# Optimization experiments

Measured on AMD Instinct MI355X. Metric: run time of the kernel, lower is better.

Reference implementation:

```python
import jax, jax.numpy as jnp
import numpy as np

LATENT = 512
VOCAB = 32000
START_TOKEN = 0
END_TOKEN = 1
BATCH = 128
BN_EPS = 1e-5


def setup_inputs() -> dict:
    key = jax.random.key(0)
    k = jax.random.split(key, 10)
    s = 0.02
    L, V = LATENT, VOCAB
    return {
        "z": jax.random.normal(k[0], (BATCH, L), dtype=jnp.float32),
        "emb": jax.random.normal(k[1], (V, L), dtype=jnp.float32) * s,      # embedding table
        "Wp1": jax.random.normal(k[2], (2 * L, L), dtype=jnp.float32) * s,  # project layer 1
        "bp1": jnp.zeros((2 * L,), jnp.float32),
        "Wp2": jax.random.normal(k[3], (2 * L, 2 * L), dtype=jnp.float32) * s,  # project layer 2
        "bp2": jnp.zeros((2 * L,), jnp.float32),
        "Wih": jax.random.normal(k[4], (4 * L, L), dtype=jnp.float32) * s,  # LSTMCell input weights (i,f,g,o)
        "Whh": jax.random.normal(k[5], (4 * L, L), dtype=jnp.float32) * s,
        "bih": jnp.zeros((4 * L,), jnp.float32),
        "bhh": jnp.zeros((4 * L,), jnp.float32),
        "Wo1": jax.random.normal(k[6], (2 * L, L), dtype=jnp.float32) * s,  # output MLP layer 1
        "bo1": jnp.zeros((2 * L,), jnp.float32),
        "bn_g": jnp.ones((2 * L,), jnp.float32),   # BatchNorm1d (eval mode)
        "bn_b": jnp.zeros((2 * L,), jnp.float32),
        "bn_m": jnp.zeros((2 * L,), jnp.float32),
        "bn_v": jnp.ones((2 * L,), jnp.float32),
        "Wo2": jax.random.normal(k[7], (V - 1, 2 * L), dtype=jnp.float32) * s,  # vocab head
        "bo2": jnp.zeros((V - 1,), jnp.float32),
        "max_len": 50,
    }


def _elu01(x):
    # nn.ELU(alpha=0.1)
    return jnp.where(x > 0, x, 0.1 * (jnp.exp(x) - 1.0))


def _run(z, emb, Wp1, bp1, Wp2, bp2, Wih, Whh, bih, bhh,
         Wo1, bo1, bn_g, bn_b, bn_m, bn_v, Wo2, bo2, max_len):
    B, L = z.shape
    # project z -> (h, c); dropout inactive in eval mode
    h1 = jax.nn.relu(z @ Wp1.T + bp1)
    hc = _elu01(h1 @ Wp2.T + bp2)
    h, c = jnp.split(hc, 2, axis=1)            # each [B, L]
    e0 = jnp.broadcast_to(emb[START_TOKEN], (B, L))
    keys = jax.random.split(jax.random.key(42), max_len)
    inv_std = bn_g / jnp.sqrt(bn_v + BN_EPS)   # fused BN scale (eval)

    def step(carry, key):
        h, c, e = carry
        gates = e @ Wih.T + bih + h @ Whh.T + bhh
        i, f, g, o = jnp.split(gates, 4, axis=1)  # torch LSTMCell gate order
        c = jax.nn.sigmoid(f) * c + jax.nn.sigmoid(i) * jnp.tanh(g)
        h = jax.nn.sigmoid(o) * jnp.tanh(c)
        a = jax.nn.relu(h) @ Wo1.T + bo1
        a = (a - bn_m) * inv_std + bn_b
        logits = jax.nn.relu(a) @ Wo2.T + bo2      # [B, V-1]
        logp = jax.nn.log_softmax(logits, axis=-1)
        # Categorical sampling via Gumbel-max
        sample = jnp.argmax(logits + jax.random.gumbel(key, logits.shape), axis=-1)
        lp = jnp.take_along_axis(logp, sample[:, None], axis=1)[:, 0]
        ent = -jnp.sum(jnp.exp(logp) * logp, axis=-1)
        return (h, c, jnp.take(emb, sample, axis=0)), (sample, lp, ent)

    _, (xs, lps, ents) = jax.lax.scan(step, (h, c, e0), keys)
    x = xs.T          # [B, T]
    lps = lps.T       # [B, T]
    ents = ents.T     # [B, T]
    # first END occurrence (argmax returns first max; replicates torch semantics incl. its length-1 quirk)
    end_pos = jnp.argmax((x == END_TOKEN).astype(jnp.float32), axis=1)
    seq_len = end_pos + 1
    seq_len = jnp.where(seq_len == 1, max_len, seq_len)
    mask = jnp.arange(max_len)[None, :] < seq_len[:, None]
    x_out = jnp.where(mask, x + 1, 0)                      # pad_sequence(padding=-1) then +1 -> 0 pad
    lp_out = jnp.where(mask, lps, 0.0)                     # padded per-step log-probs
    ent_mean = jnp.sum(jnp.where(mask, ents, 0.0), axis=1) / seq_len.astype(ents.dtype)
    return x_out, lp_out, ent_mean


def reference(z, emb, Wp1, bp1, Wp2, bp2, Wih, Whh, bih, bhh,
              Wo1, bo1, bn_g, bn_b, bn_m, bn_v, Wo2, bo2, max_len):
    return _run(z, emb, Wp1, bp1, Wp2, bp2, Wih, Whh, bih, bhh,
                Wo1, bo1, bn_g, bn_b, bn_m, bn_v, Wo2, bo2, max_len)
```

## Files before the change

kernel.cpp:

```cpp
#include <hip/hip_runtime.h>
#include <stdint.h>
#include <math.h>

#define BATCH  128
#define NV     31999
#define NSTEP  50
#define NPB    500
#define TINYF  1.17549435e-38f

typedef __attribute__((ext_vector_type(8))) short bf16x8;
typedef __attribute__((ext_vector_type(4))) float f32x4;
typedef __attribute__((ext_vector_type(4))) unsigned int u32x4;

__host__ __device__ __forceinline__ void tf2x32(uint32_t k0, uint32_t k1,
                                                uint32_t x0, uint32_t x1,
                                                uint32_t& o0, uint32_t& o1) {
  uint32_t k2 = k0 ^ k1 ^ 0x1BD11BDAu;
  x0 += k0; x1 += k1;
#define TF_R(r) { x0 += x1; x1 = (x1 << (r)) | (x1 >> (32 - (r))); x1 ^= x0; }
  TF_R(13) TF_R(15) TF_R(26) TF_R(6)
  x0 += k1; x1 += k2 + 1u;
  TF_R(17) TF_R(29) TF_R(16) TF_R(24)
  x0 += k2; x1 += k0 + 2u;
  TF_R(13) TF_R(15) TF_R(26) TF_R(6)
  x0 += k0; x1 += k1 + 3u;
  TF_R(17) TF_R(29) TF_R(16) TF_R(24)
  x0 += k1; x1 += k2 + 4u;
  TF_R(13) TF_R(15) TF_R(26) TF_R(6)
  x0 += k2; x1 += k0 + 5u;
#undef TF_R
  o0 = x0; o1 = x1;
}

__device__ __forceinline__ float sigm(float x) { return 1.0f / (1.0f + expf(-x)); }

__device__ __forceinline__ float gumbelv(uint32_t k0, uint32_t k1, uint32_t f) {
  uint32_t o0, o1; tf2x32(k0, k1, 0u, f, o0, o1);
  uint32_t bits = o0 ^ o1;
  float ff = __uint_as_float((bits >> 9) | 0x3f800000u) - 1.0f;
  float u = ff + TINYF;
  return -logf(-logf(u));
}

__device__ __forceinline__ unsigned short bfhi(float x) {
  uint32_t u = __float_as_uint(x);
  u += 0x7fffu + ((u >> 16) & 1u);
  return (unsigned short)(u >> 16);
}
__device__ __forceinline__ void split2(float x, unsigned short& h, unsigned short& l) {
  unsigned short hh = bfhi(x);
  float hf = __uint_as_float(((uint32_t)hh) << 16);
  h = hh; l = bfhi(x - hf);
}

#define MFMA3(ah, al, bh, bl, c)                                            \
  c = __builtin_amdgcn_mfma_f32_16x16x32_bf16(ah, bh, c, 0, 0, 0);          \
  c = __builtin_amdgcn_mfma_f32_16x16x32_bf16(ah, bl, c, 0, 0, 0);          \
  c = __builtin_amdgcn_mfma_f32_16x16x32_bf16(al, bh, c, 0, 0, 0);

__global__ __launch_bounds__(256) void gemm_part(
    const float* __restrict__ A, int lda,
    const float* __restrict__ Wa, const float* __restrict__ Wb,
    int ks, int K, int N, int KC, float* __restrict__ part)
{
  __shared__ float As[32][132];
  __shared__ float Ws[32][68];
  const int tx = threadIdx.x;
  const int n0 = blockIdx.x * 64;
  const int kc = blockIdx.y;
  const int cg = tx & 15, rg = tx >> 4;
  float acc[8][4] = {};
  const int kend = (kc + 1) * KC;
  for (int kk = kc * KC; kk < kend; kk += 32) {
    __syncthreads();
#pragma unroll
    for (int i = 0; i < 16; ++i) {
      int e = tx + 256 * i; int b = e >> 5, k = e & 31;
      As[k][b] = A[b * lda + kk + k];
    }
#pragma unroll
    for (int i = 0; i < 8; ++i) {
      int e = tx + 256 * i; int n = e >> 5, k = e & 31;
      int nn = n0 + n, kg = kk + k;
      float w;
      if (kg < ks) w = Wa[(size_t)nn * ks + kg];
      else         w = Wb[(size_t)nn * (K - ks) + (kg - ks)];
      Ws[k][n] = w;
    }
    __syncthreads();
#pragma unroll
    for (int k = 0; k < 32; ++k) {
      float4 a0 = *(const float4*)&As[k][rg * 8];
      float4 a1 = *(const float4*)&As[k][rg * 8 + 4];
      float4 wv = *(const float4*)&Ws[k][cg * 4];
      float ar[8] = {a0.x, a0.y, a0.z, a0.w, a1.x, a1.y, a1.z, a1.w};
      float wr[4] = {wv.x, wv.y, wv.z, wv.w};
#pragma unroll
      for (int r = 0; r < 8; ++r)
#pragma unroll
        for (int c = 0; c < 4; ++c) acc[r][c] += ar[r] * wr[c];
    }
  }
  size_t base = (size_t)kc * BATCH * N;
#pragma unroll
  for (int r = 0; r < 8; ++r) {
    int row = rg * 8 + r;
    float4 v4 = make_float4(acc[r][0], acc[r][1], acc[r][2], acc[r][3]);
    *(float4*)&part[base + (size_t)row * N + n0 + cg * 4] = v4;
  }
}

__global__ void k_reduce_relu(const float* __restrict__ part, int nkc,
                              const float* __restrict__ bias,
                              float* __restrict__ out, int N) {
  int i = blockIdx.x * 256 + threadIdx.x;
  int n = i % N;
  float s = bias[n];
  for (int kc = 0; kc < nkc; ++kc) s += part[(size_t)kc * BATCH * N + i];
  out[i] = fmaxf(s, 0.0f);
}

__global__ void k_reduce_elu_split(const float* __restrict__ part, int nkc,
                                   const float* __restrict__ bias,
                                   unsigned short* __restrict__ xh,
                                   unsigned short* __restrict__ xl,
                                   float* __restrict__ cbuf) {
  int i = blockIdx.x * 256 + threadIdx.x;
  int b = i >> 10, n = i & 1023;
  float s = bias[n];
  for (int kc = 0; kc < nkc; ++kc) s += part[(size_t)kc * BATCH * 1024 + i];
  float e = (s > 0.0f) ? s : 0.1f * (expf(s) - 1.0f);
  if (n < 512) {
    unsigned short h_, l_; split2(e, h_, l_);
    xh[b * 1024 + 512 + n] = h_; xl[b * 1024 + 512 + n] = l_;
  } else cbuf[b * 512 + (n - 512)] = e;
}

__global__ void k_fill_e0(const float* __restrict__ emb,
                          unsigned short* __restrict__ xh,
                          unsigned short* __restrict__ xl) {
  int i = blockIdx.x * 256 + threadIdx.x;
  int b = i >> 9, k = i & 511;
  unsigned short h_, l_; split2(emb[k], h_, l_);
  xh[b * 1024 + k] = h_; xl[b * 1024 + k] = l_;
}

__global__ void k_prep_gates(const float* __restrict__ Wih, const float* __restrict__ Whh,
                             const float* __restrict__ bih, const float* __restrict__ bhh,
                             unsigned short* __restrict__ Wh, unsigned short* __restrict__ Wl,
                             float* __restrict__ bg) {
  int i = blockIdx.x * 256 + threadIdx.x;
  int idx8 = i * 8;
  int n = idx8 >> 10, k0 = idx8 & 1023;
  const float* src = (k0 < 512) ? (Wih + (size_t)n * 512 + k0)
                                : (Whh + (size_t)n * 512 + (k0 - 512));
  float4 a = *(const float4*)src, b = *(const float4*)(src + 4);
  float wv[8] = {a.x, a.y, a.z, a.w, b.x, b.y, b.z, b.w};
  unsigned short hh[8], ll[8];
#pragma unroll
  for (int q = 0; q < 8; ++q) split2(wv[q], hh[q], ll[q]);
  u32x4 h4, l4;
#pragma unroll
  for (int q = 0; q < 4; ++q) {
    h4[q] = (uint32_t)hh[2 * q] | ((uint32_t)hh[2 * q + 1] << 16);
    l4[q] = (uint32_t)ll[2 * q] | ((uint32_t)ll[2 * q + 1] << 16);
  }
  *(u32x4*)(Wh + (size_t)idx8) = h4;
  *(u32x4*)(Wl + (size_t)idx8) = l4;
  if (i < 256) {
#pragma unroll
    for (int q = 0; q < 8; ++q) bg[i * 8 + q] = bih[i * 8 + q] + bhh[i * 8 + q];
  }
}

__global__ void k_prep_out1(const float* __restrict__ Wo1, const float* __restrict__ bo1,
                            const float* __restrict__ g, const float* __restrict__ bb,
                            const float* __restrict__ m, const float* __restrict__ v,
                            unsigned short* __restrict__ Wh, unsigned short* __restrict__ Wl,
                            float* __restrict__ S, float* __restrict__ T) {
  int i = blockIdx.x * 256 + threadIdx.x;
  int idx8 = i * 8;
  float4 a = *(const float4*)(Wo1 + idx8), b = *(const float4*)(Wo1 + idx8 + 4);
  float wv[8] = {a.x, a.y, a.z, a.w, b.x, b.y, b.z, b.w};
  unsigned short hh[8], ll[8];
#pragma unroll
  for (int q = 0; q < 8; ++q) split2(wv[q], hh[q], ll[q]);
  u32x4 h4, l4;
#pragma unroll
  for (int q = 0; q < 4; ++q) {
    h4[q] = (uint32_t)hh[2 * q] | ((uint32_t)hh[2 * q + 1] << 16);
    l4[q] = (uint32_t)ll[2 * q] | ((uint32_t)ll[2 * q + 1] << 16);
  }
  *(u32x4*)(Wh + (size_t)idx8) = h4;
  *(u32x4*)(Wl + (size_t)idx8) = l4;
  if (i < 128) {
#pragma unroll
    for (int q = 0; q < 8; ++q) {
      int n = i * 8 + q;
      float s = g[n] / sqrtf(v[n] + 1e-5f);
      S[n] = s;
      T[n] = (bo1[n] - m[n]) * s + bb[n];
    }
  }
}

__global__ void k_prep_wo2(const float* __restrict__ W,
                           unsigned short* __restrict__ Wh, unsigned short* __restrict__ Wl,
                           int total8) {
  int i = blockIdx.x * 256 + threadIdx.x;
  if (i >= total8) return;
  const float* wp = W + (size_t)i * 8;
  float4 a = *(const float4*)wp, b = *(const float4*)(wp + 4);
  float wv[8] = {a.x, a.y, a.z, a.w, b.x, b.y, b.z, b.w};
  unsigned short hh[8], ll[8];
#pragma unroll
  for (int q = 0; q < 8; ++q) split2(wv[q], hh[q], ll[q]);
  u32x4 h4, l4;
#pragma unroll
  for (int q = 0; q < 4; ++q) {
    h4[q] = (uint32_t)hh[2 * q] | ((uint32_t)hh[2 * q + 1] << 16);
    l4[q] = (uint32_t)ll[2 * q] | ((uint32_t)ll[2 * q + 1] << 16);
  }
  *(u32x4*)(Wh + (size_t)i * 8) = h4;
  *(u32x4*)(Wl + (size_t)i * 8) = l4;
}

__global__ __launch_bounds__(256) void k_gates(
    const unsigned short* __restrict__ Ah, const unsigned short* __restrict__ Al,
    const unsigned short* __restrict__ Wh, const unsigned short* __restrict__ Wl,
    const float* __restrict__ bg, float* __restrict__ cbuf,
    unsigned short* __restrict__ xh, unsigned short* __restrict__ xl,
    unsigned short* __restrict__ rhh, unsigned short* __restrict__ rhl)
{
  __shared__ __align__(16) unsigned char SM[40960];
  unsigned short (*WHb)[2][64][40] = (unsigned short(*)[2][64][40])SM;
  unsigned short (*WLb)[2][64][40] = (unsigned short(*)[2][64][40])(SM + 20480);
  const int tx = threadIdx.x;
  const int lane = tx & 63, w = tx >> 6;
  const int l15 = lane & 15, g4 = lane >> 4;
  const int gblk = blockIdx.x;
  const int arow0 = w * 32 + l15, ak = g4 * 8;
  const int sr = tx >> 2, sq = tx & 3;
  const int grow = (sr >> 4) * 512 + gblk * 16 + (sr & 15);
  const size_t wbase = (size_t)grow * 1024;

  f32x4 acc[2][4] = {};
  u32x4 RH[2][2], RL[2][2];
  bf16x8 QH[2][2][2], QL[2][2][2];

  auto ldW = [&](int set, int t) {
    const int kk = t * 64 + sq * 16;
    RH[set][0] = *(const u32x4*)(Wh + wbase + kk);
    RH[set][1] = *(const u32x4*)(Wh + wbase + kk + 8);
    RL[set][0] = *(const u32x4*)(Wl + wbase + kk);
    RL[set][1] = *(const u32x4*)(Wl + wbase + kk + 8);
  };
  auto stW = [&](int set, int buf) {
    const int kc = sq >> 1, ko = (sq & 1) * 16;
    *(u32x4*)&WHb[buf][kc][sr][ko]     = RH[set][0];
    *(u32x4*)&WHb[buf][kc][sr][ko + 8] = RH[set][1];
    *(u32x4*)&WLb[buf][kc][sr][ko]     = RL[set][0];
    *(u32x4*)&WLb[buf][kc][sr][ko + 8] = RL[set][1];
  };
  auto ldA = [&](int set, int t) {
#pragma unroll
    for (int rf = 0; rf < 2; ++rf)
#pragma unroll
      for (int kc = 0; kc < 2; ++kc) {
        size_t ao = (size_t)(arow0 + rf * 16) * 1024 + t * 64 + kc * 32 + ak;
        QH[set][rf][kc] = *(const bf16x8*)(Ah + ao);
        QL[set][rf][kc] = *(const bf16x8*)(Al + ao);
      }
  };
  auto comp = [&](int buf, int set) {
#pragma unroll
    for (int kc = 0; kc < 2; ++kc)
#pragma unroll
      for (int cf = 0; cf < 4; ++cf) {
        int col = cf * 16 + l15;
        bf16x8 bh = *(const bf16x8*)&WHb[buf][kc][col][ak];
        bf16x8 bl = *(const bf16x8*)&WLb[buf][kc][col][ak];
#pragma unroll
        for (int rf = 0; rf < 2; ++rf) { MFMA3(QH[set][rf][kc], QL[set][rf][kc], bh, bl, acc[rf][cf]); }
      }
  };

  ldW(0, 0); ldW(1, 1); ldA(0, 0);
  stW(0, 0); __syncthreads();
  for (int t = 0; t < 16; ++t) {
    const int pb = t & 1;
    if (t < 14) ldW(pb, t + 2);
    if (t < 15) ldA(pb ^ 1, t + 1);
    comp(pb, pb);
    if (t < 15) stW(pb ^ 1, pb ^ 1);
    __syncthreads();
  }
  float* gex = (float*)SM;
#pragma unroll
  for (int rf = 0; rf < 2; ++rf)
#pragma unroll
    for (int cf = 0; cf < 4; ++cf)
#pragma unroll
      for (int r = 0; r < 4; ++r) {
        int brow = w * 32 + rf * 16 + g4 * 4 + r;
        gex[(cf * 128 + brow) * 17 + l15] = acc[rf][cf][r];
      }
  __syncthreads();
#pragma unroll
  for (int i = 0; i < 8; ++i) {
    int e = tx + 256 * i;
    int b = e >> 4, lj = e & 15;
    int jg = gblk * 16 + lj;
    float gi = gex[(0 * 128 + b) * 17 + lj] + bg[jg];
    float gf = gex[(1 * 128 + b) * 17 + lj] + bg[512 + jg];
    float gg = gex[(2 * 128 + b) * 17 + lj] + bg[1024 + jg];
    float go = gex[(3 * 128 + b) * 17 + lj] + bg[1536 + jg];
    float co = cbuf[b * 512 + jg];
    float cn = sigm(gf) * co + sigm(gi) * tanhf(gg);
    float hn = sigm(go) * tanhf(cn);
    cbuf[b * 512 + jg] = cn;
    unsigned short h_, l_;
    split2(hn, h_, l_);
    xh[b * 1024 + 512 + jg] = h_; xl[b * 1024 + 512 + jg] = l_;
    float r = fmaxf(hn, 0.0f);
    split2(r, h_, l_);
    rhh[b * 512 + jg] = h_; rhl[b * 512 + jg] = l_;
  }
}

__global__ __launch_bounds__(256) void k_out1(
    const unsigned short* __restrict__ Ah, const unsigned short* __restrict__ Al,
    const unsigned short* __restrict__ Wh, const unsigned short* __restrict__ Wl,
    const float* __restrict__ S, const float* __restrict__ T,
    unsigned short* __restrict__ r2h, unsigned short* __restrict__ r2l)
{
  __shared__ __align__(16) unsigned char SM[40960];
  unsigned short (*WHb)[2][64][40] = (unsigned short(*)[2][64][40])SM;
  unsigned short (*WLb)[2][64][40] = (unsigned short(*)[2][64][40])(SM + 20480);
  const int tx = threadIdx.x;
  const int lane = tx & 63, w = tx >> 6;
  const int l15 = lane & 15, g4 = lane >> 4;
  const int n0 = blockIdx.x * 64;
  const int arow0 = w * 32 + l15, ak = g4 * 8;
  const int sr = tx >> 2, sq = tx & 3;
  const size_t wbase = (size_t)(n0 + sr) * 512;

  f32x4 acc[2][4] = {};
  u32x4 RH[2][2], RL[2][2];
  bf16x8 QH[2][2][2], QL[2][2][2];

  auto ldW = [&](int set, int t) {
    const int kk = t * 64 + sq * 16;
    RH[set][0] = *(const u32x4*)(Wh + wbase + kk);
    RH[set][1] = *(const u32x4*)(Wh + wbase + kk + 8);
    RL[set][0] = *(const u32x4*)(Wl + wbase + kk);
    RL[set][1] = *(const u32x4*)(Wl + wbase + kk + 8);
  };
  auto stW = [&](int set, int buf) {
    const int kc = sq >> 1, ko = (sq & 1) * 16;
    *(u32x4*)&WHb[buf][kc][sr][ko]     = RH[set][0];
    *(u32x4*)&WHb[buf][kc][sr][ko + 8] = RH[set][1];
    *(u32x4*)&WLb[buf][kc][sr][ko]     = RL[set][0];
    *(u32x4*)&WLb[buf][kc][sr][ko + 8] = RL[set][1];
  };
  auto ldA = [&](int set, int t) {
#pragma unroll
    for (int rf = 0; rf < 2; ++rf)
#pragma unroll
      for (int kc = 0; kc < 2; ++kc) {
        size_t ao = (size_t)(arow0 + rf * 16) * 512 + t * 64 + kc * 32 + ak;
        QH[set][rf][kc] = *(const bf16x8*)(Ah + ao);
        QL[set][rf][kc] = *(const bf16x8*)(Al + ao);
      }
  };
  auto comp = [&](int buf, int set) {
#pragma unroll
    for (int kc = 0; kc < 2; ++kc)
#pragma unroll
      for (int cf = 0; cf < 4; ++cf) {
        int col = cf * 16 + l15;
        bf16x8 bh = *(const bf16x8*)&WHb[buf][kc][col][ak];
        bf16x8 bl = *(const bf16x8*)&WLb[buf][kc][col][ak];
#pragma unroll
        for (int rf = 0; rf < 2; ++rf) { MFMA3(QH[set][rf][kc], QL[set][rf][kc], bh, bl, acc[rf][cf]); }
      }
  };

  ldW(0, 0); ldW(1, 1); ldA(0, 0);
  stW(0, 0); __syncthreads();
  for (int t = 0; t < 8; ++t) {
    const int pb = t & 1;
    if (t < 6) ldW(pb, t + 2);
    if (t < 7) ldA(pb ^ 1, t + 1);
    comp(pb, pb);
    if (t < 7) stW(pb ^ 1, pb ^ 1);
    __syncthreads();
  }
#pragma unroll
  for (int cf = 0; cf < 4; ++cf) {
    int n = n0 + cf * 16 + l15;
    float s = S[n], t = T[n];
#pragma unroll
    for (int rf = 0; rf < 2; ++rf)
#pragma unroll
      for (int r = 0; r < 4; ++r) {
        int row = w * 32 + rf * 16 + g4 * 4 + r;
        float v = fmaxf(acc[rf][cf][r] * s + t, 0.0f);
        unsigned short h_, l_; split2(v, h_, l_);
        r2h[row * 1024 + n] = h_; r2l[row * 1024 + n] = l_;
      }
  }
}

template<int PRE>
__global__ __launch_bounds__(512, 4) void k_vocab(
    const unsigned short* __restrict__ Ah, const unsigned short* __restrict__ Al,
    const unsigned short* __restrict__ Wh, const unsigned short* __restrict__ Wl,
    const float* __restrict__ Wf, const float* __restrict__ bias,
    uint32_t key0, uint32_t key1,
    float* __restrict__ vpmax, float* __restrict__ vps1, float* __restrict__ vps2,
    float* __restrict__ vpbv, float* __restrict__ vpbl, int* __restrict__ vpbi)
{
  __shared__ __align__(16) unsigned char SM[40960];
  unsigned short (*WHb)[2][64][40] = (unsigned short(*)[2][64][40])SM;
  unsigned short (*WLb)[2][64][40] = (unsigned short(*)[2][64][40])(SM + 20480);
  const int tx = threadIdx.x;
  const int lane = tx & 63, w = tx >> 6;
  const int l15 = lane & 15, g4 = lane >> 4;
  const int n0 = blockIdx.x * 64;
  const int arow = w * 16 + l15, ak = g4 * 8;
  const int sr = tx >> 3, sq = tx & 7;
  int grow = n0 + sr; if (grow >= NV) grow = NV - 1;
  const size_t wbase = (size_t)grow * 1024;
  const int skc = sq >> 2, sko = (sq & 3) * 8;

  f32x4 acc[4] = {};
  u32x4 RH[3], RL[3];
  float4 RF[3][2];
  bf16x8 QH[2][2], QL[2][2];

  auto ldW = [&](int s, int t) {
    const int kk = t * 64 + sq * 8;
    if (PRE) {
      RH[s] = *(const u32x4*)(Wh + wbase + kk);
      RL[s] = *(const u32x4*)(Wl + wbase + kk);
    } else {
      RF[s][0] = *(const float4*)(Wf + wbase + kk);
      RF[s][1] = *(const float4*)(Wf + wbase + kk + 4);
    }
  };
  auto stW = [&](int s, int buf) {
    if (PRE) {
      *(u32x4*)&WHb[buf][skc][sr][sko] = RH[s];
      *(u32x4*)&WLb[buf][skc][sr][sko] = RL[s];
    } else {
      float fv[8] = {RF[s][0].x, RF[s][0].y, RF[s][0].z, RF[s][0].w,
                     RF[s][1].x, RF[s][1].y, RF[s][1].z, RF[s][1].w};
      unsigned short hh[8], ll[8];
#pragma unroll
      for (int q = 0; q < 8; ++q) split2(fv[q], hh[q], ll[q]);
#pragma unroll
      for (int q = 0; q < 8; ++q) { WHb[buf][skc][sr][sko + q] = hh[q]; WLb[buf][skc][sr][sko + q] = ll[q]; }
    }
  };
  auto ldA = [&](int s, int t) {
#pragma unroll
    for (int kc = 0; kc < 2; ++kc) {
      size_t ao = (size_t)arow * 1024 + t * 64 + kc * 32 + ak;
      QH[s][kc] = *(const bf16x8*)(Ah + ao);
      QL[s][kc] = *(const bf16x8*)(Al + ao);
    }
  };
  auto comp = [&](int buf, int s) {
#pragma unroll
    for (int kc = 0; kc < 2; ++kc)
#pragma unroll
      for (int cf = 0; cf < 4; ++cf) {
        int col = cf * 16 + l15;
        bf16x8 bh = *(const bf16x8*)&WHb[buf][kc][col][ak];
        bf16x8 bl = *(const bf16x8*)&WLb[buf][kc][col][ak];
        MFMA3(QH[s][kc], QL[s][kc], bh, bl, acc[cf]);
      }
  };

  ldW(0, 0); ldW(1, 1); ldW(2, 2); ldA(0, 0);
  stW(0, 0); __syncthreads();
  for (int t = 0; t < 16; ++t) {
    const int pb = t & 1;
    if (t < 13) ldW(t % 3, t + 3);
    if (t < 15) ldA((t + 1) & 1, t + 1);
    comp(pb, t & 1);
    if (t < 15) stW((t + 1) % 3, pb ^ 1);
    __syncthreads();
  }
  float bias_c[4]; int vcol[4];
#pragma unroll
  for (int cf = 0; cf < 4; ++cf) {
    int v = n0 + cf * 16 + l15;
    vcol[cf] = v;
    bias_c[cf] = (v < NV) ? bias[v] : 0.0f;
  }
#pragma unroll
  for (int reg = 0; reg < 4; ++reg) {
    int row = w * 16 + g4 * 4 + reg;
    float lv[4], pv[4];
    float mm = -INFINITY;
#pragma unroll
    for (int cf = 0; cf < 4; ++cf) {
      if (vcol[cf] < NV) {
        float l = acc[cf][reg] + bias_c[cf];
        float g = gumbelv(key0, key1, (uint32_t)row * 31999u + (uint32_t)vcol[cf]);
        lv[cf] = l; pv[cf] = l + g;
        mm = fmaxf(mm, l);
      } else { lv[cf] = -INFINITY; pv[cf] = -INFINITY; }
    }
    for (int d = 1; d <= 8; d <<= 1) mm = fmaxf(mm, __shfl_xor(mm, d));
    float s1 = 0.0f, s2 = 0.0f;
#pragma unroll
    for (int cf = 0; cf < 4; ++cf)
      if (vcol[cf] < NV) { float t = lv[cf] - mm; float e = expf(t); s1 += e; s2 += e * t; }
    for (int d = 1; d <= 8; d <<= 1) { s1 += __shfl_xor(s1, d); s2 += __shfl_xor(s2, d); }
    float bv = -INFINITY, bl_ = 0.0f; int bi = 0x7fffffff;
#pragma unroll
    for (int cf = 0; cf < 4; ++cf)
      if (pv[cf] > bv || (pv[cf] == bv && vcol[cf] < bi)) { bv = pv[cf]; bi = vcol[cf]; bl_ = lv[cf]; }
    for (int d = 1; d <= 8; d <<= 1) {
      float ov = __shfl_xor(bv, d); int oi = __shfl_xor(bi, d); float ol = __shfl_xor(bl_, d);
      if (ov > bv || (ov == bv && oi < bi)) { bv = ov; bi = oi; bl_ = ol; }
    }
    if (l15 == 0) {
      int o = row * NPB + blockIdx.x;
      vpmax[o] = mm; vps1[o] = s1; vps2[o] = s2;
      vpbv[o] = bv; vpbl[o] = bl_; vpbi[o] = bi;
    }
  }
}

__global__ void k_final_sample(const float* __restrict__ vpmax, const float* __restrict__ vps1,
                               const float* __restrict__ vps2, const float* __restrict__ vpbv,
                               const float* __restrict__ vpbl, const int* __restrict__ vpbi,
                               int t, int* __restrict__ xhist, float* __restrict__ lph,
                               float* __restrict__ enth, const float* __restrict__ emb,
                               unsigned short* __restrict__ xh, unsigned short* __restrict__ xl) {
  int b = blockIdx.x, lane = threadIdx.x;
  float M = -INFINITY;
  for (int p = lane; p < NPB; p += 64) M = fmaxf(M, vpmax[b * NPB + p]);
  for (int d = 32; d; d >>= 1) M = fmaxf(M, __shfl_xor(M, d));
  float S1 = 0.0f, S2 = 0.0f, bv = -INFINITY, bl = 0.0f; int bi = 0x7fffffff;
  for (int p = lane; p < NPB; p += 64) {
    int o = b * NPB + p;
    float dm = vpmax[o] - M;
    float sc = expf(dm);
    S1 += vps1[o] * sc;
    S2 += (vps2[o] + dm * vps1[o]) * sc;
    float v = vpbv[o]; int ii = vpbi[o];
    if (v > bv || (v == bv && ii < bi)) { bv = v; bi = ii; bl = vpbl[o]; }
  }
  for (int d = 32; d; d >>= 1) {
    S1 += __shfl_xor(S1, d); S2 += __shfl_xor(S2, d);
    float ov = __shfl_xor(bv, d); int oi = __shfl_xor(bi, d); float ol = __shfl_xor(bl, d);
    if (ov > bv || (ov == bv && oi < bi)) { bv = ov; bi = oi; bl = ol; }
  }
  float logZ = logf(S1);
  if (lane == 0) {
    xhist[t * 128 + b] = bi;
    lph[t * 128 + b] = bl - M - logZ;
    enth[t * 128 + b] = logZ - S2 / S1;
  }
  const float* er = emb + (size_t)bi * 512;
  for (int k = lane; k < 512; k += 64) {
    unsigned short h_, l_; split2(er[k], h_, l_);
    xh[b * 1024 + k] = h_; xl[b * 1024 + k] = l_;
  }
}

__global__ void k_finalize(const int* __restrict__ xhist, const float* __restrict__ lph,
                           const float* __restrict__ enth, float* __restrict__ out) {
  int b = blockIdx.x, lane = threadIdx.x;
  int tok = -1, cand = 1 << 20;
  if (lane < NSTEP) {
    tok = xhist[lane * 128 + b];
    if (tok == 1) cand = lane;
  }
  int e = cand;
  for (int d = 32; d; d >>= 1) e = min(e, __shfl_xor(e, d));
  int end_pos = (e >= (1 << 20)) ? 0 : e;
  int seq_len = end_pos + 1;
  if (seq_len == 1) seq_len = NSTEP;
  float ent = 0.0f;
  if (lane < NSTEP) {
    bool msk = lane < seq_len;
    out[b * NSTEP + lane]        = msk ? (float)(tok + 1) : 0.0f;
    out[6400 + b * NSTEP + lane] = msk ? lph[lane * 128 + b] : 0.0f;
    ent = msk ? enth[lane * 128 + b] : 0.0f;
  }
  for (int d = 32; d; d >>= 1) ent += __shfl_xor(ent, d);
  if (lane == 0) out[12800 + b] = ent / (float)seq_len;
}

extern "C" void kernel_launch(void* const* d_in, const int* in_sizes, int n_in,
                              void* d_out, int out_size, void* d_ws, size_t ws_size,
                              hipStream_t stream) {
  const float* z    = (const float*)d_in[0];
  const float* emb  = (const float*)d_in[1];
  const float* Wp1  = (const float*)d_in[2];
  const float* bp1  = (const float*)d_in[3];
  const float* Wp2  = (const float*)d_in[4];
  const float* bp2  = (const float*)d_in[5];
  const float* Wih  = (const float*)d_in[6];
  const float* Whh  = (const float*)d_in[7];
  const float* bih  = (const float*)d_in[8];
  const float* bhh  = (const float*)d_in[9];
  const float* Wo1  = (const float*)d_in[10];
  const float* bo1  = (const float*)d_in[11];
  const float* bng  = (const float*)d_in[12];
  const float* bnb  = (const float*)d_in[13];
  const float* bnm  = (const float*)d_in[14];
  const float* bnv  = (const float*)d_in[15];
  const float* Wo2  = (const float*)d_in[16];
  const float* bo2  = (const float*)d_in[17];
  float* out = (float*)d_out;
  (void)in_sizes; (void)n_in; (void)out_size;

  char* base = (char*)d_ws;
  size_t off = 0;
  auto alloc = [&](size_t bytes) -> void* {
    void* p = base + off;
    off = (off + bytes + 255) & ~(size_t)255;
    return p;
  };
  unsigned short* xh[2]; unsigned short* xl[2];
  xh[0] = (unsigned short*)alloc(128 * 1024 * 2);
  xl[0] = (unsigned short*)alloc(128 * 1024 * 2);
  xh[1] = (unsigned short*)alloc(128 * 1024 * 2);
  xl[1] = (unsigned short*)alloc(128 * 1024 * 2);
  float* cbuf = (float*)alloc(128 * 512 * 4);
  unsigned short* rhh = (unsigned short*)alloc(128 * 512 * 2);
  unsigned short* rhl = (unsigned short*)alloc(128 * 512 * 2);
  unsigned short* r2h = (unsigned short*)alloc(128 * 1024 * 2);
  unsigned short* r2l = (unsigned short*)alloc(128 * 1024 * 2);
  float* h1    = (float*)alloc(128 * 1024 * 4);
  float* apart = (float*)alloc((size_t)8 * 128 * 1024 * 4);
  unsigned short* Wgh = (unsigned short*)alloc((size_t)2048 * 1024 * 2);
  unsigned short* Wgl = (unsigned short*)alloc((size_t)2048 * 1024 * 2);
  float* bg = (float*)alloc(2048 * 4);
  unsigned short* Wo1h = (unsigned short*)alloc((size_t)1024 * 512 * 2);
  unsigned short* Wo1l = (unsigned short*)alloc((size_t)1024 * 512 * 2);
  float* Sbn = (float*)alloc(1024 * 4);
  float* Tbn = (float*)alloc(1024 * 4);
  float* vpmax = (float*)alloc((size_t)NPB * 128 * 4);
  float* vps1  = (float*)alloc((size_t)NPB * 128 * 4);
  float* vps2  = (float*)alloc((size_t)NPB * 128 * 4);
  float* vpbv  = (float*)alloc((size_t)NPB * 128 * 4);
  float* vpbl  = (float*)alloc((size_t)NPB * 128 * 4);
  int*   vpbi  = (int*)alloc((size_t)NPB * 128 * 4);
  int*   xhist = (int*)alloc(50 * 128 * 4);
  float* lph   = (float*)alloc(50 * 128 * 4);
  float* enth  = (float*)alloc(50 * 128 * 4);
  size_t wo2_elems = (size_t)NV * 1024;
  bool pre = ws_size >= off + 2 * wo2_elems * 2 + (1 << 20);
  unsigned short* Wo2h = nullptr; unsigned short* Wo2l = nullptr;
  if (pre) {
    Wo2h = (unsigned short*)alloc(wo2_elems * 2);
    Wo2l = (unsigned short*)alloc(wo2_elems * 2);
  }

  uint32_t outk[100];
  for (int t = 0; t < 50; ++t) {
    uint32_t y0, y1;
    tf2x32(0u, 42u, 0u, (uint32_t)t, y0, y1);
    outk[2 * t] = y0; outk[2 * t + 1] = y1;
  }

  k_prep_gates<<<1024, 256, 0, stream>>>(Wih, Whh, bih, bhh, Wgh, Wgl, bg);
  k_prep_out1<<<256, 256, 0, stream>>>(Wo1, bo1, bng, bnb, bnm, bnv, Wo1h, Wo1l, Sbn, Tbn);
  if (pre) {
    int total8 = (int)(wo2_elems / 8);
    k_prep_wo2<<<(total8 + 255) / 256, 256, 0, stream>>>(Wo2, Wo2h, Wo2l, total8);
  }

  k_fill_e0<<<256, 256, 0, stream>>>(emb, xh[0], xl[0]);
  gemm_part<<<dim3(16, 4), 256, 0, stream>>>(z, 512, Wp1, Wp1, 512, 512, 1024, 128, apart);
  k_reduce_relu<<<512, 256, 0, stream>>>(apart, 4, bp1, h1, 1024);
  gemm_part<<<dim3(16, 8), 256, 0, stream>>>(h1, 1024, Wp2, Wp2, 1024, 1024, 1024, 128, apart);
  k_reduce_elu_split<<<512, 256, 0, stream>>>(apart, 8, bp2, xh[0], xl[0], cbuf);

  for (int t = 0; t < NSTEP; ++t) {
    int ri = t & 1, wi = ri ^ 1;
    k_gates<<<32, 256, 0, stream>>>(xh[ri], xl[ri], Wgh, Wgl, bg, cbuf,
                                    xh[wi], xl[wi], rhh, rhl);
    k_out1<<<16, 256, 0, stream>>>(rhh, rhl, Wo1h, Wo1l, Sbn, Tbn, r2h, r2l);
    if (pre)
      k_vocab<1><<<NPB, 512, 0, stream>>>(r2h, r2l, Wo2h, Wo2l, Wo2, bo2,
                                          outk[2 * t], outk[2 * t + 1],
                                          vpmax, vps1, vps2, vpbv, vpbl, vpbi);
    else
      k_vocab<0><<<NPB, 512, 0, stream>>>(r2h, r2l, nullptr, nullptr, Wo2, bo2,
                                          outk[2 * t], outk[2 * t + 1],
                                          vpmax, vps1, vps2, vpbv, vpbl, vpbi);
    k_final_sample<<<128, 64, 0, stream>>>(vpmax, vps1, vps2, vpbv, vpbl, vpbi,
                                           t, xhist, lph, enth, emb, xh[wi], xl[wi]);
  }
  k_finalize<<<128, 64, 0, stream>>>(xhist, lph, enth, out);
}
```

Before: 4.828 ms.

## Load vocab weights straight to registers, dropping LDS staging and block barriers

The vocab-head GEMM kernel no longer stages weight tiles through shared memory with __syncthreads. Each lane now loads its MFMA B fragments directly from global memory into a two-stage register double buffer. The 4-blocks-per-SM launch bound hint is also removed. This removes LDS traffic and barriers, but each weight row is now fetched separately by every wave in the block (8x more global/L2 reads). Uncoalesced 16-byte strided loads and higher register pressure may lower occupancy.

```diff
diff --git a/kernel.cpp b/kernel.cpp
--- a/kernel.cpp
+++ b/kernel.cpp
@@ -413,7 +413,7 @@
 }
 
 template<int PRE>
-__global__ __launch_bounds__(512, 4) void k_vocab(
+__global__ __launch_bounds__(512) void k_vocab(
     const unsigned short* __restrict__ Ah, const unsigned short* __restrict__ Al,
     const unsigned short* __restrict__ Wh, const unsigned short* __restrict__ Wl,
     const float* __restrict__ Wf, const float* __restrict__ bias,
@@ -421,77 +421,77 @@
     float* __restrict__ vpmax, float* __restrict__ vps1, float* __restrict__ vps2,
     float* __restrict__ vpbv, float* __restrict__ vpbl, int* __restrict__ vpbi)
 {
-  __shared__ __align__(16) unsigned char SM[40960];
-  unsigned short (*WHb)[2][64][40] = (unsigned short(*)[2][64][40])SM;
-  unsigned short (*WLb)[2][64][40] = (unsigned short(*)[2][64][40])(SM + 20480);
   const int tx = threadIdx.x;
   const int lane = tx & 63, w = tx >> 6;
   const int l15 = lane & 15, g4 = lane >> 4;
   const int n0 = blockIdx.x * 64;
-  const int arow = w * 16 + l15, ak = g4 * 8;
-  const int sr = tx >> 3, sq = tx & 7;
-  int grow = n0 + sr; if (grow >= NV) grow = NV - 1;
-  const size_t wbase = (size_t)grow * 1024;
-  const int skc = sq >> 2, sko = (sq & 3) * 8;
+  const int arow = w * 16 + l15;
+  const int ko = g4 * 8;
+  const size_t abase = (size_t)arow * 1024 + ko;
+  size_t wr4[4];
+#pragma unroll
+  for (int cf = 0; cf < 4; ++cf) {
+    int v = n0 + cf * 16 + l15;
+    if (v >= NV) v = NV - 1;
+    wr4[cf] = (size_t)v * 1024 + ko;
+  }
 
   f32x4 acc[4] = {};
-  u32x4 RH[3], RL[3];
-  float4 RF[3][2];
-  bf16x8 QH[2][2], QL[2][2];
-
-  auto ldW = [&](int s, int t) {
-    const int kk = t * 64 + sq * 8;
+  bf16x8 BH0[4], BL0[4], BH1[4], BL1[4], AH0, AL0, AH1, AL1;
+
+  auto ld0 = [&](int step) {
+    const int kk = step * 32;
+    AH0 = *(const bf16x8*)(Ah + abase + kk);
+    AL0 = *(const bf16x8*)(Al + abase + kk);
     if (PRE) {
-      RH[s] = *(const u32x4*)(Wh + wbase + kk);
-      RL[s] = *(const u32x4*)(Wl + wbase + kk);
+#pragma unroll
+      for (int cf = 0; cf < 4; ++cf) {
+        BH0[cf] = *(const bf16x8*)(Wh + wr4[cf] + kk);
+        BL0[cf] = *(const bf16x8*)(Wl + wr4[cf] + kk);
+      }
     } else {
-      RF[s][0] = *(const float4*)(Wf + wbase + kk);
-      RF[s][1] = *(const float4*)(Wf + wbase + kk + 4);
-    }
-  };
-  auto stW = [&](int s, int buf) {
+#pragma unroll
+      for (int cf = 0; cf < 4; ++cf) {
+        const float* wp = Wf + wr4[cf] + kk;
+        float4 f0 = *(const float4*)wp, f1 = *(const float4*)(wp + 4);
+        float fv[8] = {f0.x, f0.y, f0.z, f0.w, f1.x, f1.y, f1.z, f1.w};
+        short* bh = (short*)&BH0[cf]; short* bl = (short*)&BL0[cf];
+#pragma unroll
+        for (int q = 0; q < 8; ++q) { unsigned short h_, l_; split2(fv[q], h_, l_); bh[q] = (short)h_; bl[q] = (short)l_; }
+      }
+    }
+  };
+  auto ld1 = [&](int step) {
+    const int kk = step * 32;
+    AH1 = *(const bf16x8*)(Ah + abase + kk);
+    AL1 = *(const bf16x8*)(Al + abase + kk);
     if (PRE) {
-      *(u32x4*)&WHb[buf][skc][sr][sko] = RH[s];
-      *(u32x4*)&WLb[buf][skc][sr][sko] = RL[s];
+#pragma unroll
+      for (int cf = 0; cf < 4; ++cf) {
+        BH1[cf] = *(const bf16x8*)(Wh + wr4[cf] + kk);
+        BL1[cf] = *(const bf16x8*)(Wl + wr4[cf] + kk);
+      }
     } else {
-      float fv[8] = {RF[s][0].x, RF[s][0].y, RF[s][0].z, RF[s][0].w,
-                     RF[s][1].x, RF[s][1].y, RF[s][1].z, RF[s][1].w};
-      unsigned short hh[8], ll[8];
-#pragma unroll
-      for (int q = 0; q < 8; ++q) split2(fv[q], hh[q], ll[q]);
-#pragma unroll
-      for (int q = 0; q < 8; ++q) { WHb[buf][skc][sr][sko + q] = hh[q]; WLb[buf][skc][sr][sko + q] = ll[q]; }
-    }
-  };
-  auto ldA = [&](int s, int t) {
-#pragma unroll
-    for (int kc = 0; kc < 2; ++kc) {
-      size_t ao = (size_t)arow * 1024 + t * 64 + kc * 32 + ak;
-      QH[s][kc] = *(const bf16x8*)(Ah + ao);
-      QL[s][kc] = *(const bf16x8*)(Al + ao);
-    }
-  };
-  auto comp = [&](int buf, int s) {
-#pragma unroll
-    for (int kc = 0; kc < 2; ++kc)
 #pragma unroll
       for (int cf = 0; cf < 4; ++cf) {
-        int col = cf * 16 + l15;
-        bf16x8 bh = *(const bf16x8*)&WHb[buf][kc][col][ak];
-        bf16x8 bl = *(const bf16x8*)&WLb[buf][kc][col][ak];
-        MFMA3(QH[s][kc], QL[s][kc], bh, bl, acc[cf]);
-      }
-  };
-
-  ldW(0, 0); ldW(1, 1); ldW(2, 2); ldA(0, 0);
-  stW(0, 0); __syncthreads();
-  for (int t = 0; t < 16; ++t) {
-    const int pb = t & 1;
-    if (t < 13) ldW(t % 3, t + 3);
-    if (t < 15) ldA((t + 1) & 1, t + 1);
-    comp(pb, t & 1);
-    if (t < 15) stW((t + 1) % 3, pb ^ 1);
-    __syncthreads();
+        const float* wp = Wf + wr4[cf] + kk;
+        float4 f0 = *(const float4*)wp, f1 = *(const float4*)(wp + 4);
+        float fv[8] = {f0.x, f0.y, f0.z, f0.w, f1.x, f1.y, f1.z, f1.w};
+        short* bh = (short*)&BH1[cf]; short* bl = (short*)&BL1[cf];
+#pragma unroll
+        for (int q = 0; q < 8; ++q) { unsigned short h_, l_; split2(fv[q], h_, l_); bh[q] = (short)h_; bl[q] = (short)l_; }
+      }
+    }
+  };
+
+  ld0(0); ld1(1);
+  for (int step = 0; step < 32; step += 2) {
+#pragma unroll
+    for (int cf = 0; cf < 4; ++cf) { MFMA3(AH0, AL0, BH0[cf], BL0[cf], acc[cf]); }
+    if (step < 30) ld0(step + 2);
+#pragma unroll
+    for (int cf = 0; cf < 4; ++cf) { MFMA3(AH1, AL1, BH1[cf], BL1[cf], acc[cf]); }
+    if (step < 30) ld1(step + 3);
   }
   float bias_c[4]; int vcol[4];
 #pragma unroll
```

New measurement: 9.960 ms. 106% more time.
